# Kernel optimization log

Hardware: AMD Instinct MI355X
Metric: run time of the kernel (lower is better)

## Reference

```python
import jax, jax.numpy as jnp
import numpy as np

MARGIN = 0.3


def _l2norm(x, axis=-1):
    return x / (jnp.linalg.norm(x, axis=axis, keepdims=True) + 1e-12)


def setup_inputs() -> dict:
    key = jax.random.key(0)
    k1, k2, k3, k4 = jax.random.split(key, 4)
    n, P, d = 1024, 8, 2048
    global_feat = jax.random.normal(k1, (n, d), dtype=jnp.float32)
    partial_feat = jax.random.normal(k2, (n, P, d), dtype=jnp.float32)
    part_labels = jax.random.randint(k3, (n, P), 0, 2).astype(jnp.float32)
    global_labels = jax.random.randint(k4, (n,), 0, 64).astype(jnp.int64)
    return {"global_feat": global_feat, "partial_feat": partial_feat,
            "part_labels": part_labels, "global_labels": global_labels}


def reference(global_feat, partial_feat, part_labels, global_labels):
    # --- compute_distance (VGTripletLoss) ---
    g = _l2norm(global_feat)            # [n, d]
    p = _l2norm(partial_feat)           # [n, P, d]
    gs = (1.0 - g @ g.T) / 2.0          # [n, n]
    overlap = part_labels[:, None, :] * part_labels[None, :, :]   # [n, n, P]
    # per-part cosine distance: [n, n, P]
    slf = (1.0 - jnp.einsum('ipd,jpd->ijp', p, p)) / 2.0
    slf = slf * overlap
    dist = (slf.sum(-1) + gs) / (overlap.sum(-1) + 1.0)            # [n, n]

    # --- compute_loss: hard positive/negative mining ---
    mask = global_labels[:, None] == global_labels[None, :]        # [n, n]
    neg_inf = jnp.float32(-1e30)
    pos_inf = jnp.float32(1e30)
    dist_ap = jnp.max(jnp.where(mask, dist, neg_inf), axis=1)      # hardest positive
    dist_an = jnp.min(jnp.where(mask, pos_inf, dist), axis=1)      # hardest negative
    # MarginRankingLoss(y=1, reduction='mean'): max(0, dist_ap - dist_an + margin)
    loss = jnp.mean(jax.nn.relu(dist_ap - dist_an + MARGIN))
    return loss
```

## Files before the change

### kernel.cpp

```cpp
#include <hip/hip_runtime.h>

#define N 1024
#define D 2048
#define P 8
#define F 9
#define KTOT (F * D)
#define SPLIT 8
#define KS (KTOT / SPLIT)
#define BM 128
#define BKT 32
#define MARGIN 0.3f

typedef float f32x4 __attribute__((ext_vector_type(4)));
typedef short s16x8 __attribute__((ext_vector_type(8)));

#define GLOBAL_AS __attribute__((address_space(1)))
#define LDS_AS __attribute__((address_space(3)))

__device__ __forceinline__ const float* feat_row(const float* __restrict__ g,
                                                 const float* __restrict__ p,
                                                 int i, int f) {
    return (f == 0) ? (g + (size_t)i * D)
                    : (p + ((size_t)i * P + (f - 1)) * D);
}

__device__ __forceinline__ unsigned f2bf(float x) {
    unsigned u = __float_as_uint(x);
    return (u + 0x7fffu + ((u >> 16) & 1u)) >> 16;
}

__global__ void pack_kernel(const float* __restrict__ gfeat,
                            const float* __restrict__ pfeat,
                            const float* __restrict__ plab,
                            unsigned short* __restrict__ V) {
    const int r = blockIdx.x;
    const int i = r / F, f = r % F;
    const float* src = feat_row(gfeat, pfeat, i, f);
    const int t = threadIdx.x;
    const float4* s4 = (const float4*)src;
    float4 a = s4[2 * t];
    float4 b = s4[2 * t + 1];
    float ss = a.x*a.x + a.y*a.y + a.z*a.z + a.w*a.w
             + b.x*b.x + b.y*b.y + b.z*b.z + b.w*b.w;
    __shared__ float red[256];
    __shared__ float invs;
    red[t] = ss;
    __syncthreads();
    for (int s = 128; s > 0; s >>= 1) {
        if (t < s) red[t] += red[t + s];
        __syncthreads();
    }
    if (t == 0) {
        float ls = (f == 0) ? 1.0f : plab[i * P + (f - 1)];
        invs = ls / (sqrtf(red[0]) + 1e-12f);
    }
    __syncthreads();
    const float inv = invs;
    uint4 o;
    o.x = f2bf(a.x * inv) | (f2bf(a.y * inv) << 16);
    o.y = f2bf(a.z * inv) | (f2bf(a.w * inv) << 16);
    o.z = f2bf(b.x * inv) | (f2bf(b.y * inv) << 16);
    o.w = f2bf(b.z * inv) | (f2bf(b.w * inv) << 16);
    *(uint4*)&V[(size_t)r * D + t * 8] = o;
}

__global__ __launch_bounds__(256)
void gemm_kernel(const unsigned short* __restrict__ V,
                 float* __restrict__ part) {
    __shared__ short As[BM * BKT];
    __shared__ short Bs[BM * BKT];

    const int t = threadIdx.x;
    const int wave = t >> 6, lane = t & 63;
    const int i0 = blockIdx.y * BM;
    const int j0 = blockIdx.x * BM;
    const int kbase = blockIdx.z * KS;

    const unsigned short* Ap = V + (size_t)(i0 + (t >> 2)) * KTOT + kbase + (t & 3) * 8;
    const unsigned short* Bp = V + (size_t)(j0 + (t >> 2)) * KTOT + kbase + (t & 3) * 8;

    const int kq = lane >> 4;
    const short* Abase = As + ((wave & 1) * 64 + (lane & 15)) * BKT + kq * 8;
    const short* Bbase = Bs + ((wave >> 1) * 64 + (lane & 15)) * BKT + kq * 8;

    f32x4 acc[4][4];
    #pragma unroll
    for (int m = 0; m < 4; ++m)
        #pragma unroll
        for (int n = 0; n < 4; ++n)
            acc[m][n] = (f32x4){0.f, 0.f, 0.f, 0.f};

    for (int ks = 0; ks < KS / BKT; ++ks) {
        __syncthreads();
        __builtin_amdgcn_global_load_lds((const GLOBAL_AS void*)Ap,
                                         (LDS_AS void*)(As + t * 8), 16, 0, 0);
        __builtin_amdgcn_global_load_lds((const GLOBAL_AS void*)(Ap + (size_t)64 * KTOT),
                                         (LDS_AS void*)(As + 2048 + t * 8), 16, 0, 0);
        __builtin_amdgcn_global_load_lds((const GLOBAL_AS void*)Bp,
                                         (LDS_AS void*)(Bs + t * 8), 16, 0, 0);
        __builtin_amdgcn_global_load_lds((const GLOBAL_AS void*)(Bp + (size_t)64 * KTOT),
                                         (LDS_AS void*)(Bs + 2048 + t * 8), 16, 0, 0);
        Ap += BKT;
        Bp += BKT;
        __syncthreads();

        s16x8 af[4], bf[4];
        #pragma unroll
        for (int m = 0; m < 4; ++m) af[m] = *(const s16x8*)(Abase + m * 16 * BKT);
        #pragma unroll
        for (int n = 0; n < 4; ++n) bf[n] = *(const s16x8*)(Bbase + n * 16 * BKT);
        #pragma unroll
        for (int m = 0; m < 4; ++m)
            #pragma unroll
            for (int n = 0; n < 4; ++n)
                acc[m][n] = __builtin_amdgcn_mfma_f32_16x16x32_bf16(
                    af[m], bf[n], acc[m][n], 0, 0, 0);
    }

    float* outp = part + (size_t)blockIdx.z * N * N;
    const int rbase = i0 + (wave & 1) * 64 + (lane >> 4) * 4;
    const int cbase = j0 + (wave >> 1) * 64 + (lane & 15);
    #pragma unroll
    for (int m = 0; m < 4; ++m)
        #pragma unroll
        for (int n = 0; n < 4; ++n)
            #pragma unroll
            for (int r = 0; r < 4; ++r)
                outp[(size_t)(rbase + m * 16 + r) * N + cbase + n * 16] = acc[m][n][r];
}

__global__ void mine_kernel(const float* __restrict__ part,
                            const float* __restrict__ plab,
                            const int* __restrict__ glab,
                            float* __restrict__ rowloss) {
    const int i = blockIdx.x;
    const int t = threadIdx.x;
    const int li = glab[i];
    float lab_i[P];
    #pragma unroll
    for (int c = 0; c < P; ++c) lab_i[c] = plab[i * P + c];

    float ap = -1e30f, an = 1e30f;
    for (int j = t; j < N; j += 256) {
        float dot = 0.f;
        #pragma unroll
        for (int s = 0; s < SPLIT; ++s)
            dot += part[(size_t)s * N * N + (size_t)i * N + j];
        float ov = 0.f;
        #pragma unroll
        for (int c = 0; c < P; ++c) ov += lab_i[c] * plab[j * P + c];
        float d = 0.5f - dot / (2.0f * (ov + 1.0f));
        if (glab[j] == li) ap = fmaxf(ap, d);
        else               an = fminf(an, d);
    }
    __shared__ float smax[256], smin[256];
    smax[t] = ap; smin[t] = an;
    __syncthreads();
    for (int s = 128; s > 0; s >>= 1) {
        if (t < s) {
            smax[t] = fmaxf(smax[t], smax[t + s]);
            smin[t] = fminf(smin[t], smin[t + s]);
        }
        __syncthreads();
    }
    if (t == 0) rowloss[i] = fmaxf(0.f, smax[0] - smin[0] + MARGIN);
}

__global__ void reduce_kernel(const float* __restrict__ rowloss,
                              float* __restrict__ out) {
    const int t = threadIdx.x;
    float s = rowloss[t] + rowloss[t + 256] + rowloss[t + 512] + rowloss[t + 768];
    __shared__ float red[256];
    red[t] = s;
    __syncthreads();
    for (int st = 128; st > 0; st >>= 1) {
        if (t < st) red[t] += red[t + st];
        __syncthreads();
    }
    if (t == 0) out[0] = red[0] * (1.0f / N);
}

extern "C" void kernel_launch(void* const* d_in, const int* in_sizes, int n_in,
                              void* d_out, int out_size, void* d_ws, size_t ws_size,
                              hipStream_t stream) {
    const float* gfeat = (const float*)d_in[0];
    const float* pfeat = (const float*)d_in[1];
    const float* plab  = (const float*)d_in[2];
    const int*   glab  = (const int*)d_in[3];
    float* out = (float*)d_out;

    char* ws = (char*)d_ws;
    unsigned short* V = (unsigned short*)ws;
    float* part    = (float*)(ws + (size_t)37748736);
    float* rowloss = (float*)(ws + (size_t)37748736 + 33554432);

    pack_kernel<<<N * F, 256, 0, stream>>>(gfeat, pfeat, plab, V);
    gemm_kernel<<<dim3(N / BM, N / BM, SPLIT), 256, 0, stream>>>(V, part);
    mine_kernel<<<N, 256, 0, stream>>>(part, plab, glab, rowloss);
    reduce_kernel<<<1, 256, 0, stream>>>(rowloss, out);
}
```

Measured before the change: 174.0 us.

## Use wave-per-row pack, XCD-aware GEMM block remap, and adaptive split-K

The pack kernel now normalizes one feature row per wavefront, using a shuffle reduction instead of a 256-thread shared-memory reduction with many barriers. The GEMM remaps linear workgroup ids so consecutive tiles land on the same XCD, which should improve L2 reuse of shared A/B panels. When the workspace is large enough, split-K rises from 8 to 16 to launch more workgroups on the many-CU device. The cost is twice the partial-sum traffic written and then read back by the mining kernel, whose split loop is no longer unrolled.

```diff
diff --git a/kernel.cpp b/kernel.cpp
--- a/kernel.cpp
+++ b/kernel.cpp
@@ -5,8 +5,6 @@
 #define P 8
 #define F 9
 #define KTOT (F * D)
-#define SPLIT 8
-#define KS (KTOT / SPLIT)
 #define BM 128
 #define BKT 32
 #define MARGIN 0.3f
@@ -29,52 +27,58 @@
     return (u + 0x7fffu + ((u >> 16) & 1u)) >> 16;
 }
 
-__global__ void pack_kernel(const float* __restrict__ gfeat,
-                            const float* __restrict__ pfeat,
-                            const float* __restrict__ plab,
-                            unsigned short* __restrict__ V) {
-    const int r = blockIdx.x;
-    const int i = r / F, f = r % F;
+__global__ __launch_bounds__(256)
+void pack_kernel(const float* __restrict__ gfeat,
+                 const float* __restrict__ pfeat,
+                 const float* __restrict__ plab,
+                 unsigned short* __restrict__ V) {
+    const int wid = (blockIdx.x << 2) | (threadIdx.x >> 6);
+    const int lane = threadIdx.x & 63;
+    const int i = wid / F, f = wid % F;
     const float* src = feat_row(gfeat, pfeat, i, f);
-    const int t = threadIdx.x;
     const float4* s4 = (const float4*)src;
-    float4 a = s4[2 * t];
-    float4 b = s4[2 * t + 1];
-    float ss = a.x*a.x + a.y*a.y + a.z*a.z + a.w*a.w
-             + b.x*b.x + b.y*b.y + b.z*b.z + b.w*b.w;
-    __shared__ float red[256];
-    __shared__ float invs;
-    red[t] = ss;
-    __syncthreads();
-    for (int s = 128; s > 0; s >>= 1) {
-        if (t < s) red[t] += red[t + s];
-        __syncthreads();
-    }
-    if (t == 0) {
-        float ls = (f == 0) ? 1.0f : plab[i * P + (f - 1)];
-        invs = ls / (sqrtf(red[0]) + 1e-12f);
-    }
-    __syncthreads();
-    const float inv = invs;
-    uint4 o;
-    o.x = f2bf(a.x * inv) | (f2bf(a.y * inv) << 16);
-    o.y = f2bf(a.z * inv) | (f2bf(a.w * inv) << 16);
-    o.z = f2bf(b.x * inv) | (f2bf(b.y * inv) << 16);
-    o.w = f2bf(b.z * inv) | (f2bf(b.w * inv) << 16);
-    *(uint4*)&V[(size_t)r * D + t * 8] = o;
+    float4 a[8];
+    #pragma unroll
+    for (int q = 0; q < 8; ++q) a[q] = s4[q * 64 + lane];
+    float ss = 0.f;
+    #pragma unroll
+    for (int q = 0; q < 8; ++q)
+        ss += a[q].x * a[q].x + a[q].y * a[q].y + a[q].z * a[q].z + a[q].w * a[q].w;
+    #pragma unroll
+    for (int m = 32; m > 0; m >>= 1) ss += __shfl_xor(ss, m, 64);
+    const float ls = (f == 0) ? 1.0f : plab[i * P + (f - 1)];
+    const float inv = ls / (sqrtf(ss) + 1e-12f);
+    unsigned short* dst = V + (size_t)wid * D;
+    #pragma unroll
+    for (int q = 0; q < 8; ++q) {
+        uint2 o;
+        o.x = f2bf(a[q].x * inv) | (f2bf(a[q].y * inv) << 16);
+        o.y = f2bf(a[q].z * inv) | (f2bf(a[q].w * inv) << 16);
+        *(uint2*)&dst[(q * 64 + lane) * 4] = o;
+    }
 }
 
 __global__ __launch_bounds__(256)
 void gemm_kernel(const unsigned short* __restrict__ V,
-                 float* __restrict__ part) {
+                 float* __restrict__ part, int ks) {
     __shared__ short As[BM * BKT];
     __shared__ short Bs[BM * BKT];
 
+    const int nwg = gridDim.x * gridDim.y * gridDim.z;
+    const int l = blockIdx.x + gridDim.x * (blockIdx.y + gridDim.y * blockIdx.z);
+    const int q = nwg >> 3;
+    const int wg = (l & 7) * q + (l >> 3);
+    const int bx = wg & 7;
+    const int rem = wg >> 3;
+    const int by = rem & 7;
+    const int bz = rem >> 3;
+
     const int t = threadIdx.x;
     const int wave = t >> 6, lane = t & 63;
-    const int i0 = blockIdx.y * BM;
-    const int j0 = blockIdx.x * BM;
-    const int kbase = blockIdx.z * KS;
+    const int i0 = by * BM;
+    const int j0 = bx * BM;
+    const int kbase = bz * ks;
+    const int nsteps = ks >> 5;
 
     const unsigned short* Ap = V + (size_t)(i0 + (t >> 2)) * KTOT + kbase + (t & 3) * 8;
     const unsigned short* Bp = V + (size_t)(j0 + (t >> 2)) * KTOT + kbase + (t & 3) * 8;
@@ -90,7 +94,7 @@
         for (int n = 0; n < 4; ++n)
             acc[m][n] = (f32x4){0.f, 0.f, 0.f, 0.f};
 
-    for (int ks = 0; ks < KS / BKT; ++ks) {
+    for (int ksi = 0; ksi < nsteps; ++ksi) {
         __syncthreads();
         __builtin_amdgcn_global_load_lds((const GLOBAL_AS void*)Ap,
                                          (LDS_AS void*)(As + t * 8), 16, 0, 0);
@@ -117,7 +121,7 @@
                     af[m], bf[n], acc[m][n], 0, 0, 0);
     }
 
-    float* outp = part + (size_t)blockIdx.z * N * N;
+    float* outp = part + (size_t)bz * N * N;
     const int rbase = i0 + (wave & 1) * 64 + (lane >> 4) * 4;
     const int cbase = j0 + (wave >> 1) * 64 + (lane & 15);
     #pragma unroll
@@ -132,7 +136,7 @@
 __global__ void mine_kernel(const float* __restrict__ part,
                             const float* __restrict__ plab,
                             const int* __restrict__ glab,
-                            float* __restrict__ rowloss) {
+                            float* __restrict__ rowloss, int S) {
     const int i = blockIdx.x;
     const int t = threadIdx.x;
     const int li = glab[i];
@@ -143,8 +147,7 @@
     float ap = -1e30f, an = 1e30f;
     for (int j = t; j < N; j += 256) {
         float dot = 0.f;
-        #pragma unroll
-        for (int s = 0; s < SPLIT; ++s)
+        for (int s = 0; s < S; ++s)
             dot += part[(size_t)s * N * N + (size_t)i * N + j];
         float ov = 0.f;
         #pragma unroll
@@ -189,13 +192,19 @@
     const int*   glab  = (const int*)d_in[3];
     float* out = (float*)d_out;
 
+    const size_t vbytes = (size_t)N * KTOT * 2;
+    const size_t slice  = (size_t)N * N * 4;
+
+    int S = (ws_size != 0 && ws_size >= vbytes + 16 * slice + 4096) ? 16 : 8;
+    const int ks = KTOT / S;
+
     char* ws = (char*)d_ws;
     unsigned short* V = (unsigned short*)ws;
-    float* part    = (float*)(ws + (size_t)37748736);
-    float* rowloss = (float*)(ws + (size_t)37748736 + 33554432);
-
-    pack_kernel<<<N * F, 256, 0, stream>>>(gfeat, pfeat, plab, V);
-    gemm_kernel<<<dim3(N / BM, N / BM, SPLIT), 256, 0, stream>>>(V, part);
-    mine_kernel<<<N, 256, 0, stream>>>(part, plab, glab, rowloss);
+    float* part    = (float*)(ws + vbytes);
+    float* rowloss = (float*)(ws + vbytes + (size_t)S * slice);
+
+    pack_kernel<<<N * F / 4, 256, 0, stream>>>(gfeat, pfeat, plab, V);
+    gemm_kernel<<<dim3(N / BM, N / BM, S), 256, 0, stream>>>(V, part, ks);
+    mine_kernel<<<N, 256, 0, stream>>>(part, plab, glab, rowloss, S);
     reduce_kernel<<<1, 256, 0, stream>>>(rowloss, out);
 }
```

New measurement: 182.3 us. 1.05x slower.
